# Kernel tuning notes

Hardware: AMD Instinct MI355X
Metric: run time of the kernel (lower is better)

Reference implementation:

```python
import jax, jax.numpy as jnp
import numpy as np

M, K, E, N, TOPK = 4096, 1024, 8, 1024, 2

def setup_inputs() -> dict:
    key = jax.random.key(0)
    k1, k2, k3, k4, k5 = jax.random.split(key, 5)
    hidden_states = jax.random.normal(k1, (M, K), dtype=jnp.float32)
    w1 = jax.random.normal(k2, (E, K, 2 * N), dtype=jnp.float32) * 0.02
    w2 = jax.random.normal(k3, (E, N, K), dtype=jnp.float32) * 0.02
    topk_weights = jax.random.uniform(k4, (M, TOPK), dtype=jnp.float32)
    topk_ids = jax.random.randint(k5, (M, TOPK), 0, E, dtype=jnp.int64)
    return {"hidden_states": hidden_states, "w1": w1, "w2": w2,
            "topk_weights": topk_weights, "topk_ids": topk_ids}

def reference(hidden_states, w1, w2, topk_weights, topk_ids):
    # Fused MoE: per expert e, y_e = silu_and_mul(x @ w1[e]) @ w2[e];
    # output[m] = sum_k topk_weights[m,k] * y_{topk_ids[m,k]}[m]
    num_experts = w1.shape[0]
    n = w2.shape[1]

    def expert_step(acc, inputs):
        w1_e, w2_e, e = inputs
        gate_up = hidden_states @ w1_e            # [M, 2N]
        gate, up = gate_up[:, :n], gate_up[:, n:]
        h = jax.nn.silu(gate) * up                 # [M, N]
        y_e = h @ w2_e                             # [M, K]
        # combined routing weight of expert e per token (scatter-free finalize)
        coef = jnp.sum(jnp.where(topk_ids == e, topk_weights, 0.0), axis=1)  # [M]
        return acc + coef[:, None] * y_e, None

    init = jnp.zeros_like(hidden_states)
    out, _ = jax.lax.scan(expert_step, init,
                          (w1, w2, jnp.arange(num_experts, dtype=topk_ids.dtype)))
    return out
```

## Files before the change

### kernel.cpp

```cpp
#include <hip/hip_runtime.h>


#define M_TOK   4096
#define K_DIM   1024
#define N_DIM   1024
#define E_NUM   8
#define NPAIR   8192
#define BM      128
#define ROWS_CAP 9216
#define NROWBLK 72

typedef unsigned short u16;
typedef unsigned int   u32;
typedef __attribute__((ext_vector_type(8))) short bf16x8;
typedef __attribute__((ext_vector_type(4))) float f32x4;

#define GPTR(p) ((const __attribute__((address_space(1))) u32*)(const void*)(p))
#define LPTR(p) ((__attribute__((address_space(3))) u32*)(void*)(p))

__device__ __forceinline__ u16 f2bf(float f) {
  union { float f; u32 u; } v; v.f = f;
  u32 r = v.u + 0x7FFFu + ((v.u >> 16) & 1u);
  return (u16)(r >> 16);
}
__device__ __forceinline__ float bf2f(u16 u) {
  union { u32 u; float f; } v; v.u = ((u32)u) << 16;
  return v.f;
}

__device__ __forceinline__ void transpose_tile64(
    const float* __restrict__ src, u16* __restrict__ dst, int R, int Cc,
    int rb, int cb, void* shm) {
  float* lds = (float*)shm;
  const int r0 = rb * 64, c0 = cb * 64;
  const int t = threadIdx.x;
#pragma unroll
  for (int it = 0; it < 4; ++it) {
    int lin = it * 256 + t;
    int rr = lin >> 4, c4 = (lin & 15) << 2;
    float4 v = *(const float4*)&src[(size_t)(r0 + rr) * Cc + c0 + c4];
    lds[rr * 67 + c4 + 0] = v.x; lds[rr * 67 + c4 + 1] = v.y;
    lds[rr * 67 + c4 + 2] = v.z; lds[rr * 67 + c4 + 3] = v.w;
  }
  __syncthreads();
#pragma unroll
  for (int it = 0; it < 4; ++it) {
    int lin = it * 256 + t;
    int cc = lin >> 4, r4 = (lin & 15) << 2;
    ushort4 o;
    o.x = f2bf(lds[(r4 + 0) * 67 + cc]);
    o.y = f2bf(lds[(r4 + 1) * 67 + cc]);
    o.z = f2bf(lds[(r4 + 2) * 67 + cc]);
    o.w = f2bf(lds[(r4 + 3) * 67 + cc]);
    *(ushort4*)&dst[(size_t)(c0 + cc) * R + r0 + r4] = o;
  }
}

__global__ __launch_bounds__(256) void prep_route_kernel(
    const float* __restrict__ hs, const float* __restrict__ w1,
    const float* __restrict__ w2, const int* __restrict__ topk_ids,
    u16* __restrict__ hsb, u16* __restrict__ w1t, u16* __restrict__ w2t,
    int* __restrict__ pair_token, int* __restrict__ pos_of,
    int* __restrict__ block_expert) {
  __shared__ __align__(16) char shm[17408];
  const int bid = blockIdx.x;
  const int t = threadIdx.x;
  if (bid == 0) {
    int* lcnt = (int*)shm;
    __shared__ int cnt[E_NUM], off[E_NUM], pad[E_NUM];
    int c[E_NUM];
#pragma unroll
    for (int e = 0; e < E_NUM; ++e) c[e] = 0;
    for (int i = 0; i < 32; ++i) c[topk_ids[t * 32 + i] & 7]++;
#pragma unroll
    for (int e = 0; e < E_NUM; ++e) lcnt[t * 8 + e] = c[e];
    __syncthreads();
    if (t < E_NUM) {
      int run = 0;
      for (int i = 0; i < 256; ++i) {
        int v = lcnt[i * 8 + t]; lcnt[i * 8 + t] = run; run += v;
      }
      cnt[t] = run;
    }
    __syncthreads();
    if (t == 0) {
      int run = 0, blk = 0;
      for (int e = 0; e < E_NUM; ++e) {
        off[e] = run;
        int padded = ((cnt[e] + BM - 1) / BM) * BM;
        pad[e] = padded;
        for (int b = 0; b < padded / BM; ++b) block_expert[blk++] = e;
        run += padded;
      }
      for (; blk < NROWBLK; ++blk) block_expert[blk] = -1;
    }
    __syncthreads();
    for (int i = 0; i < 32; ++i) {
      int p = t * 32 + i;
      int e = topk_ids[p] & 7;
      int idx = t * 8 + e;
      int pos = off[e] + lcnt[idx];
      lcnt[idx] = lcnt[idx] + 1;
      pair_token[pos] = p >> 1;
      pos_of[p] = pos;
    }
    for (int e = 0; e < E_NUM; ++e) {
      int s = off[e] + cnt[e], epos = off[e] + pad[e];
      for (int r = s + t; r < epos; r += 256) pair_token[r] = 0;
    }
  } else if (bid <= 4096) {
    int i = (bid - 1) * 256 + t;
    float4 v = ((const float4*)hs)[i];
    ushort4 o;
    o.x = f2bf(v.x); o.y = f2bf(v.y); o.z = f2bf(v.z); o.w = f2bf(v.w);
    ((ushort4*)hsb)[i] = o;
  } else if (bid <= 8192) {
    int idx = bid - 4097;
    int e = idx >> 9, rem = idx & 511;
    int cb = rem >> 4, rb = rem & 15;
    transpose_tile64(w1 + (size_t)e * 1024 * 2048, w1t + (size_t)e * 1024 * 2048,
                     1024, 2048, rb, cb, shm);
  } else {
    int idx = bid - 8193;
    int e = idx >> 8, rem = idx & 255;
    int cb = rem >> 4, rb = rem & 15;
    transpose_tile64(w2 + (size_t)e * 1024 * 1024, w2t + (size_t)e * 1024 * 1024,
                     1024, 1024, rb, cb, shm);
  }
}

template <bool GATHER, int NB>
__global__ __launch_bounds__(256, NB == 2 ? 2 : 3) void gemm128(
    const u16* __restrict__ A, const u16* __restrict__ Bt, u16* __restrict__ Out,
    const int* __restrict__ pair_token, const int* __restrict__ block_expert) {
  const int bx = ((int)blockIdx.x & 7) * (NROWBLK / 8) + ((int)blockIdx.x >> 3);
  const int e = block_expert[bx];
  if (e < 0) return;
  __shared__ __align__(16) u16 As[128 * 64];
  __shared__ __align__(16) u16 Bs[NB * 128 * 64];
  const int tid = threadIdx.x;
  const int wave = tid >> 6;
  const int lane = tid & 63;
  const int wr = wave >> 1;
  const int wc = wave & 1;
  const int srow = wave * 8 + (lane >> 3);
  const int kc = ((lane & 7) ^ (srow & 7)) << 3;

  const u16* ap[4];
#pragma unroll
  for (int is = 0; is < 4; ++is) {
    int rt = is * 32 + srow;
    int grow = bx * BM + rt;
    int arow = GATHER ? pair_token[grow] : grow;
    ap[is] = A + (size_t)arow * K_DIM + kc;
  }
  const u16* bp[NB][4];
  const u16* base_e = Bt + (size_t)e * (NB * N_DIM) * K_DIM;
#pragma unroll
  for (int nb = 0; nb < NB; ++nb)
#pragma unroll
    for (int is = 0; is < 4; ++is) {
      int n = nb * N_DIM + blockIdx.y * 128 + is * 32 + srow;
      bp[nb][is] = base_e + (size_t)n * K_DIM + kc;
    }
  u16* alds = As + wave * 512;
  u16* blds = Bs + wave * 512;

  f32x4 acc[NB][4][4];
#pragma unroll
  for (int nb = 0; nb < NB; ++nb)
#pragma unroll
    for (int i = 0; i < 4; ++i)
#pragma unroll
      for (int j = 0; j < 4; ++j) acc[nb][i][j] = f32x4{0.f, 0.f, 0.f, 0.f};

  for (int k0 = 0; k0 < K_DIM; k0 += 64) {
#pragma unroll
    for (int is = 0; is < 4; ++is)
      __builtin_amdgcn_global_load_lds(GPTR(ap[is] + k0), LPTR(alds + is * 2048), 16, 0, 0);
#pragma unroll
    for (int nb = 0; nb < NB; ++nb)
#pragma unroll
      for (int is = 0; is < 4; ++is)
        __builtin_amdgcn_global_load_lds(GPTR(bp[nb][is] + k0), LPTR(blds + nb * 8192 + is * 2048), 16, 0, 0);
    __syncthreads();
#pragma unroll
    for (int ks = 0; ks < 2; ++ks) {
      const int cq = ks * 4 + (lane >> 4);
      bf16x8 af[4], bfr[NB][4];
#pragma unroll
      for (int i = 0; i < 4; ++i) {
        int row = wr * 64 + i * 16 + (lane & 15);
        af[i] = *(const bf16x8*)&As[row * 64 + ((cq ^ (row & 7)) << 3)];
      }
#pragma unroll
      for (int nb = 0; nb < NB; ++nb)
#pragma unroll
        for (int j = 0; j < 4; ++j) {
          int n = wc * 64 + j * 16 + (lane & 15);
          bfr[nb][j] = *(const bf16x8*)&Bs[nb * 8192 + n * 64 + ((cq ^ (n & 7)) << 3)];
        }
#pragma unroll
      for (int nb = 0; nb < NB; ++nb)
#pragma unroll
        for (int i = 0; i < 4; ++i)
#pragma unroll
          for (int j = 0; j < 4; ++j)
            acc[nb][i][j] = __builtin_amdgcn_mfma_f32_16x16x32_bf16(af[i], bfr[nb][j], acc[nb][i][j], 0, 0, 0);
    }
    __syncthreads();
  }

  const size_t rbase = (size_t)bx * BM + wr * 64 + ((lane >> 4) * 4);
  const int cbase = blockIdx.y * 128 + wc * 64 + (lane & 15);
#pragma unroll
  for (int i = 0; i < 4; ++i)
#pragma unroll
    for (int j = 0; j < 4; ++j)
#pragma unroll
      for (int r = 0; r < 4; ++r) {
        float v;
        if (NB == 2) {
          float g = acc[0][i][j][r], u = acc[1][i][j][r];
          v = g * u / (1.f + __expf(-g));
        } else {
          v = acc[0][i][j][r];
        }
        Out[(rbase + i * 16 + r) * N_DIM + cbase + j * 16] = f2bf(v);
      }
}

__global__ __launch_bounds__(256) void gather_kernel(
    const u16* __restrict__ y, const float* __restrict__ tw,
    const int* __restrict__ pos_of, float* __restrict__ out) {
  int m = blockIdx.x;
  int k = threadIdx.x * 4;
  int p0 = pos_of[m * 2 + 0], p1 = pos_of[m * 2 + 1];
  float w0 = tw[m * 2 + 0], w1 = tw[m * 2 + 1];
  ushort4 y0 = *(const ushort4*)&y[(size_t)p0 * 1024 + k];
  ushort4 y1 = *(const ushort4*)&y[(size_t)p1 * 1024 + k];
  float4 o;
  o.x = w0 * bf2f(y0.x) + w1 * bf2f(y1.x);
  o.y = w0 * bf2f(y0.y) + w1 * bf2f(y1.y);
  o.z = w0 * bf2f(y0.z) + w1 * bf2f(y1.z);
  o.w = w0 * bf2f(y0.w) + w1 * bf2f(y1.w);
  *(float4*)&out[(size_t)m * 1024 + k] = o;
}

extern "C" void kernel_launch(void* const* d_in, const int* in_sizes, int n_in,
                              void* d_out, int out_size, void* d_ws, size_t ws_size,
                              hipStream_t stream) {
  const float* hs = (const float*)d_in[0];
  const float* w1 = (const float*)d_in[1];
  const float* w2 = (const float*)d_in[2];
  const float* tw = (const float*)d_in[3];
  const int* tids = (const int*)d_in[4];
  float* out = (float*)d_out;

  char* ws = (char*)d_ws;
  u16* hsb = (u16*)(ws);
  u16* w1t = (u16*)(ws + (size_t)(8u << 20));
  u16* w2t = (u16*)(ws + (size_t)(40u << 20));
  u16* h   = (u16*)(ws + (size_t)(56u << 20));
  u16* y   = (u16*)(ws + (size_t)(76u << 20));
  int* pair_token   = (int*)(ws + (size_t)(96u << 20));
  int* pos_of       = (int*)(ws + (size_t)(96u << 20) + 64 * 1024);
  int* block_expert = (int*)(ws + (size_t)(96u << 20) + 128 * 1024);

  prep_route_kernel<<<10241, 256, 0, stream>>>(
      hs, w1, w2, tids, hsb, w1t, w2t, pair_token, pos_of, block_expert);
  gemm128<true, 2><<<dim3(NROWBLK, 8), 256, 0, stream>>>(hsb, w1t, h, pair_token, block_expert);
  gemm128<false, 1><<<dim3(NROWBLK, 8), 256, 0, stream>>>(h, w2t, y, pair_token, block_expert);
  gather_kernel<<<4096, 256, 0, stream>>>(y, tw, pos_of, out);
}
```

Before: 237.1 us.

## Fuse routing-weighted combine into second GEMM epilogue via atomic scatter-add

Removes the separate gather kernel and the bf16 intermediate y buffer. The second GEMM now scales each row by its routing coefficient and atomically adds into the fp32 output at the token row. The output is zeroed in the prep kernel and the coefficients are stored per sorted position. This saves one launch and the y write and read traffic, at the cost of 16M scalar fp32 atomics that contend on tokens whose two experts land in concurrent blocks. Accumulation order also becomes nondeterministic.

```diff
diff --git a/kernel.cpp b/kernel.cpp
--- a/kernel.cpp
+++ b/kernel.cpp
@@ -58,9 +58,11 @@
 
 __global__ __launch_bounds__(256) void prep_route_kernel(
     const float* __restrict__ hs, const float* __restrict__ w1,
-    const float* __restrict__ w2, const int* __restrict__ topk_ids,
+    const float* __restrict__ w2, const float* __restrict__ tw,
+    const int* __restrict__ topk_ids,
     u16* __restrict__ hsb, u16* __restrict__ w1t, u16* __restrict__ w2t,
-    int* __restrict__ pair_token, int* __restrict__ pos_of,
+    float* __restrict__ outf,
+    int* __restrict__ pair_token, float* __restrict__ coef_of,
     int* __restrict__ block_expert) {
   __shared__ __align__(16) char shm[17408];
   const int bid = blockIdx.x;
@@ -102,11 +104,11 @@
       int pos = off[e] + lcnt[idx];
       lcnt[idx] = lcnt[idx] + 1;
       pair_token[pos] = p >> 1;
-      pos_of[p] = pos;
+      coef_of[pos] = tw[p];
     }
     for (int e = 0; e < E_NUM; ++e) {
       int s = off[e] + cnt[e], epos = off[e] + pad[e];
-      for (int r = s + t; r < epos; r += 256) pair_token[r] = 0;
+      for (int r = s + t; r < epos; r += 256) { pair_token[r] = 0; coef_of[r] = 0.f; }
     }
   } else if (bid <= 4096) {
     int i = (bid - 1) * 256 + t;
@@ -114,6 +116,7 @@
     ushort4 o;
     o.x = f2bf(v.x); o.y = f2bf(v.y); o.z = f2bf(v.z); o.w = f2bf(v.w);
     ((ushort4*)hsb)[i] = o;
+    ((float4*)outf)[i] = float4{0.f, 0.f, 0.f, 0.f};
   } else if (bid <= 8192) {
     int idx = bid - 4097;
     int e = idx >> 9, rem = idx & 511;
@@ -129,10 +132,11 @@
   }
 }
 
-template <bool GATHER, int NB>
+template <bool GATHER, int NB, bool SCATTER>
 __global__ __launch_bounds__(256, NB == 2 ? 2 : 3) void gemm128(
     const u16* __restrict__ A, const u16* __restrict__ Bt, u16* __restrict__ Out,
-    const int* __restrict__ pair_token, const int* __restrict__ block_expert) {
+    const int* __restrict__ pair_token, const int* __restrict__ block_expert,
+    const float* __restrict__ coef_of, float* __restrict__ outf) {
   const int bx = ((int)blockIdx.x & 7) * (NROWBLK / 8) + ((int)blockIdx.x >> 3);
   const int e = block_expert[bx];
   if (e < 0) return;
@@ -213,38 +217,36 @@
 
   const size_t rbase = (size_t)bx * BM + wr * 64 + ((lane >> 4) * 4);
   const int cbase = blockIdx.y * 128 + wc * 64 + (lane & 15);
-#pragma unroll
-  for (int i = 0; i < 4; ++i)
-#pragma unroll
-    for (int j = 0; j < 4; ++j)
+  if constexpr (SCATTER) {
+#pragma unroll
+    for (int i = 0; i < 4; ++i)
 #pragma unroll
       for (int r = 0; r < 4; ++r) {
-        float v;
-        if (NB == 2) {
-          float g = acc[0][i][j][r], u = acc[1][i][j][r];
-          v = g * u / (1.f + __expf(-g));
-        } else {
-          v = acc[0][i][j][r];
+        const int row = (int)rbase + i * 16 + r;
+        const int tok = pair_token[row];
+        const float cf = coef_of[row];
+        float* orow = outf + (size_t)tok * N_DIM + cbase;
+#pragma unroll
+        for (int j = 0; j < 4; ++j)
+          atomicAdd(&orow[j * 16], cf * acc[0][i][j][r]);
+      }
+  } else {
+#pragma unroll
+    for (int i = 0; i < 4; ++i)
+#pragma unroll
+      for (int j = 0; j < 4; ++j)
+#pragma unroll
+        for (int r = 0; r < 4; ++r) {
+          float v;
+          if (NB == 2) {
+            float g = acc[0][i][j][r], u = acc[1][i][j][r];
+            v = g * u / (1.f + __expf(-g));
+          } else {
+            v = acc[0][i][j][r];
+          }
+          Out[(rbase + i * 16 + r) * N_DIM + cbase + j * 16] = f2bf(v);
         }
-        Out[(rbase + i * 16 + r) * N_DIM + cbase + j * 16] = f2bf(v);
-      }
-}
-
-__global__ __launch_bounds__(256) void gather_kernel(
-    const u16* __restrict__ y, const float* __restrict__ tw,
-    const int* __restrict__ pos_of, float* __restrict__ out) {
-  int m = blockIdx.x;
-  int k = threadIdx.x * 4;
-  int p0 = pos_of[m * 2 + 0], p1 = pos_of[m * 2 + 1];
-  float w0 = tw[m * 2 + 0], w1 = tw[m * 2 + 1];
-  ushort4 y0 = *(const ushort4*)&y[(size_t)p0 * 1024 + k];
-  ushort4 y1 = *(const ushort4*)&y[(size_t)p1 * 1024 + k];
-  float4 o;
-  o.x = w0 * bf2f(y0.x) + w1 * bf2f(y1.x);
-  o.y = w0 * bf2f(y0.y) + w1 * bf2f(y1.y);
-  o.z = w0 * bf2f(y0.z) + w1 * bf2f(y1.z);
-  o.w = w0 * bf2f(y0.w) + w1 * bf2f(y1.w);
-  *(float4*)&out[(size_t)m * 1024 + k] = o;
+  }
 }
 
 extern "C" void kernel_launch(void* const* d_in, const int* in_sizes, int n_in,
@@ -262,14 +264,14 @@
   u16* w1t = (u16*)(ws + (size_t)(8u << 20));
   u16* w2t = (u16*)(ws + (size_t)(40u << 20));
   u16* h   = (u16*)(ws + (size_t)(56u << 20));
-  u16* y   = (u16*)(ws + (size_t)(76u << 20));
   int* pair_token   = (int*)(ws + (size_t)(96u << 20));
-  int* pos_of       = (int*)(ws + (size_t)(96u << 20) + 64 * 1024);
+  float* coef_of    = (float*)(ws + (size_t)(96u << 20) + 64 * 1024);
   int* block_expert = (int*)(ws + (size_t)(96u << 20) + 128 * 1024);
 
   prep_route_kernel<<<10241, 256, 0, stream>>>(
-      hs, w1, w2, tids, hsb, w1t, w2t, pair_token, pos_of, block_expert);
-  gemm128<true, 2><<<dim3(NROWBLK, 8), 256, 0, stream>>>(hsb, w1t, h, pair_token, block_expert);
-  gemm128<false, 1><<<dim3(NROWBLK, 8), 256, 0, stream>>>(h, w2t, y, pair_token, block_expert);
-  gather_kernel<<<4096, 256, 0, stream>>>(y, tw, pos_of, out);
-}
+      hs, w1, w2, tw, tids, hsb, w1t, w2t, out, pair_token, coef_of, block_expert);
+  gemm128<true, 2, false><<<dim3(NROWBLK, 8), 256, 0, stream>>>(
+      hsb, w1t, h, pair_token, block_expert, nullptr, nullptr);
+  gemm128<false, 1, true><<<dim3(NROWBLK, 8), 256, 0, stream>>>(
+      h, w2t, nullptr, pair_token, block_expert, coef_of, out);
+}
```

Result: slower. 292.4 us (+23.3%).

## Triple-buffer GEMM LDS with vmcnt-counted waits and 512-thread blocks

Applied to the files above, without the earlier changes.

Both expert GEMMs now keep three LDS stages filled by direct global-to-LDS loads issued two K-tiles ahead. Each step waits only on the vmcnt of the older stages before a raw barrier, instead of waiting for all loads at every iteration. Blocks grow to 8 waves, each computing a 64x32 slice, so each wave holds fewer accumulators and more waves hide latency. The cost is much larger dynamic LDS (up to 144 KB for the gate/up GEMM), which limits how many blocks fit per CU. The hand-written waitcnt values must exactly match the number of loads issued per stage.

```diff
diff --git a/kernel.cpp b/kernel.cpp
--- a/kernel.cpp
+++ b/kernel.cpp
@@ -17,6 +17,7 @@
 
 #define GPTR(p) ((const __attribute__((address_space(1))) u32*)(const void*)(p))
 #define LPTR(p) ((__attribute__((address_space(3))) u32*)(void*)(p))
+#define VMW(n) asm volatile("s_waitcnt vmcnt(" #n ")" ::: "memory")
 
 __device__ __forceinline__ u16 f2bf(float f) {
   union { float f; u32 u; } v; v.f = f;
@@ -130,93 +131,123 @@
 }
 
 template <bool GATHER, int NB>
-__global__ __launch_bounds__(256, NB == 2 ? 2 : 3) void gemm128(
+__global__ __launch_bounds__(512, 2) void gemm_cnt(
     const u16* __restrict__ A, const u16* __restrict__ Bt, u16* __restrict__ Out,
     const int* __restrict__ pair_token, const int* __restrict__ block_expert) {
+  constexpr int AE = 128 * 64;
+  constexpr int BE = NB * 128 * 64;
+  constexpr int KT = K_DIM / 64;
+
   const int bx = ((int)blockIdx.x & 7) * (NROWBLK / 8) + ((int)blockIdx.x >> 3);
   const int e = block_expert[bx];
   if (e < 0) return;
-  __shared__ __align__(16) u16 As[128 * 64];
-  __shared__ __align__(16) u16 Bs[NB * 128 * 64];
+  const int by = blockIdx.y;
+
+  extern __shared__ __align__(16) u16 smem[];
+  u16* As = smem;
+  u16* Bs = smem + 3 * AE;
+
   const int tid = threadIdx.x;
   const int wave = tid >> 6;
   const int lane = tid & 63;
-  const int wr = wave >> 1;
-  const int wc = wave & 1;
+  const int wr  = wave >> 2;
+  const int wcc = wave & 3;
   const int srow = wave * 8 + (lane >> 3);
   const int kc = ((lane & 7) ^ (srow & 7)) << 3;
 
-  const u16* ap[4];
-#pragma unroll
-  for (int is = 0; is < 4; ++is) {
-    int rt = is * 32 + srow;
+  const u16* ap[2];
+#pragma unroll
+  for (int is = 0; is < 2; ++is) {
+    int rt = is * 64 + srow;
     int grow = bx * BM + rt;
     int arow = GATHER ? pair_token[grow] : grow;
     ap[is] = A + (size_t)arow * K_DIM + kc;
   }
-  const u16* bp[NB][4];
+  const u16* bp[NB * 2];
   const u16* base_e = Bt + (size_t)e * (NB * N_DIM) * K_DIM;
 #pragma unroll
+  for (int is = 0; is < NB * 2; ++is) {
+    int rt = is * 64 + srow;
+    int nb = rt >> 7;
+    int n = nb * N_DIM + by * 128 + (rt & 127);
+    bp[is] = base_e + (size_t)n * K_DIM + kc;
+  }
+
+#define STAGE(buf, koff) do { \
+    _Pragma("unroll") \
+    for (int is_ = 0; is_ < 2; ++is_) \
+      __builtin_amdgcn_global_load_lds(GPTR(ap[is_] + (koff)), \
+          LPTR(&As[(buf) * AE + is_ * 4096 + wave * 512]), 16, 0, 0); \
+    _Pragma("unroll") \
+    for (int is_ = 0; is_ < NB * 2; ++is_) \
+      __builtin_amdgcn_global_load_lds(GPTR(bp[is_] + (koff)), \
+          LPTR(&Bs[(buf) * BE + is_ * 4096 + wave * 512]), 16, 0, 0); \
+  } while (0)
+
+  f32x4 acc[NB][4][2];
+#pragma unroll
   for (int nb = 0; nb < NB; ++nb)
 #pragma unroll
-    for (int is = 0; is < 4; ++is) {
-      int n = nb * N_DIM + blockIdx.y * 128 + is * 32 + srow;
-      bp[nb][is] = base_e + (size_t)n * K_DIM + kc;
-    }
-  u16* alds = As + wave * 512;
-  u16* blds = Bs + wave * 512;
-
-  f32x4 acc[NB][4][4];
-#pragma unroll
-  for (int nb = 0; nb < NB; ++nb)
-#pragma unroll
     for (int i = 0; i < 4; ++i)
 #pragma unroll
-      for (int j = 0; j < 4; ++j) acc[nb][i][j] = f32x4{0.f, 0.f, 0.f, 0.f};
-
-  for (int k0 = 0; k0 < K_DIM; k0 += 64) {
-#pragma unroll
-    for (int is = 0; is < 4; ++is)
-      __builtin_amdgcn_global_load_lds(GPTR(ap[is] + k0), LPTR(alds + is * 2048), 16, 0, 0);
-#pragma unroll
-    for (int nb = 0; nb < NB; ++nb)
-#pragma unroll
-      for (int is = 0; is < 4; ++is)
-        __builtin_amdgcn_global_load_lds(GPTR(bp[nb][is] + k0), LPTR(blds + nb * 8192 + is * 2048), 16, 0, 0);
-    __syncthreads();
+      for (int j = 0; j < 2; ++j) acc[nb][i][j] = f32x4{0.f, 0.f, 0.f, 0.f};
+
+  STAGE(0, 0);
+  STAGE(1, 64);
+
+  int cur = 0, nxt = 2;
+  for (int t = 0; t < KT; ++t) {
+    if (t < KT - 2) STAGE(nxt, (t + 2) * 64);
+    if constexpr (NB == 2) {
+      if (t < KT - 2) VMW(12);
+      else if (t == KT - 2) VMW(6);
+      else VMW(0);
+    } else {
+      if (t < KT - 2) VMW(8);
+      else if (t == KT - 2) VMW(4);
+      else VMW(0);
+    }
+    __builtin_amdgcn_s_barrier();
+    __builtin_amdgcn_sched_barrier(0);
+    const u16* Ab = &As[cur * AE];
+    const u16* Bb = &Bs[cur * BE];
 #pragma unroll
     for (int ks = 0; ks < 2; ++ks) {
       const int cq = ks * 4 + (lane >> 4);
-      bf16x8 af[4], bfr[NB][4];
+      bf16x8 af[4], bfr[NB][2];
 #pragma unroll
       for (int i = 0; i < 4; ++i) {
         int row = wr * 64 + i * 16 + (lane & 15);
-        af[i] = *(const bf16x8*)&As[row * 64 + ((cq ^ (row & 7)) << 3)];
+        af[i] = *(const bf16x8*)&Ab[row * 64 + ((cq ^ (row & 7)) << 3)];
       }
 #pragma unroll
       for (int nb = 0; nb < NB; ++nb)
 #pragma unroll
-        for (int j = 0; j < 4; ++j) {
-          int n = wc * 64 + j * 16 + (lane & 15);
-          bfr[nb][j] = *(const bf16x8*)&Bs[nb * 8192 + n * 64 + ((cq ^ (n & 7)) << 3)];
+        for (int j = 0; j < 2; ++j) {
+          int n = wcc * 32 + j * 16 + (lane & 15);
+          bfr[nb][j] = *(const bf16x8*)&Bb[nb * 8192 + n * 64 + ((cq ^ (n & 7)) << 3)];
         }
 #pragma unroll
       for (int nb = 0; nb < NB; ++nb)
 #pragma unroll
         for (int i = 0; i < 4; ++i)
 #pragma unroll
-          for (int j = 0; j < 4; ++j)
+          for (int j = 0; j < 2; ++j)
             acc[nb][i][j] = __builtin_amdgcn_mfma_f32_16x16x32_bf16(af[i], bfr[nb][j], acc[nb][i][j], 0, 0, 0);
     }
-    __syncthreads();
-  }
+    __builtin_amdgcn_s_barrier();
+    __builtin_amdgcn_sched_barrier(0);
+    cur = (cur == 2) ? 0 : cur + 1;
+    nxt = (nxt == 2) ? 0 : nxt + 1;
+  }
+#undef STAGE
 
   const size_t rbase = (size_t)bx * BM + wr * 64 + ((lane >> 4) * 4);
-  const int cbase = blockIdx.y * 128 + wc * 64 + (lane & 15);
+  const int cbase = by * 128 + wcc * 32 + (lane & 15);
 #pragma unroll
   for (int i = 0; i < 4; ++i)
 #pragma unroll
-    for (int j = 0; j < 4; ++j)
+    for (int j = 0; j < 2; ++j)
 #pragma unroll
       for (int r = 0; r < 4; ++r) {
         float v;
@@ -267,9 +298,13 @@
   int* pos_of       = (int*)(ws + (size_t)(96u << 20) + 64 * 1024);
   int* block_expert = (int*)(ws + (size_t)(96u << 20) + 128 * 1024);
 
+  size_t lds1 = (size_t)3 * (128 * 64 + 2 * 128 * 64) * sizeof(u16);
+  size_t lds2 = (size_t)3 * (128 * 64 + 1 * 128 * 64) * sizeof(u16);
   prep_route_kernel<<<10241, 256, 0, stream>>>(
       hs, w1, w2, tids, hsb, w1t, w2t, pair_token, pos_of, block_expert);
-  gemm128<true, 2><<<dim3(NROWBLK, 8), 256, 0, stream>>>(hsb, w1t, h, pair_token, block_expert);
-  gemm128<false, 1><<<dim3(NROWBLK, 8), 256, 0, stream>>>(h, w2t, y, pair_token, block_expert);
+  gemm_cnt<true, 2><<<dim3(NROWBLK, 8), 512, lds1, stream>>>(
+      hsb, w1t, h, pair_token, block_expert);
+  gemm_cnt<false, 1><<<dim3(NROWBLK, 8), 512, lds2, stream>>>(
+      h, w2t, y, pair_token, block_expert);
   gather_kernel<<<4096, 256, 0, stream>>>(y, tw, pos_of, out);
 }
```

Measured after the change: 246.2 us. 1.04x slower.
